# Performance work log

Hardware: AMD Instinct MI355X
Metric: run time of the kernel (lower is better)

The kernel has to match this reference:

```python
import jax, jax.numpy as jnp
import numpy as np

NEG_SLOPE = 0.2  # PyG GATConv default LeakyReLU slope


def add_self_loops(edge_index, n):
    loops = jnp.arange(n, dtype=edge_index.dtype)
    return jnp.concatenate([edge_index, jnp.stack([loops, loops])], axis=1)


def segment_softmax(e, seg, n):
    # e: [E, H], seg: [E] destination node ids
    m = jax.ops.segment_max(e, seg, num_segments=n)          # [N, H]
    ex = jnp.exp(e - m[seg])
    s = jax.ops.segment_sum(ex, seg, num_segments=n)          # [N, H]
    return ex / (s[seg] + 1e-16)


def gat_conv(x, edge_index, W, att_src, att_dst, bias, heads, concat):
    n = x.shape[0]
    c = W.shape[1] // heads
    ei = add_self_loops(edge_index, n)
    src, dst = ei[0], ei[1]
    h = (x @ W).reshape(n, heads, c)                          # [N, H, C]
    a_src = jnp.einsum('nhc,hc->nh', h, att_src)              # [N, H]
    a_dst = jnp.einsum('nhc,hc->nh', h, att_dst)
    e = a_src[src] + a_dst[dst]                               # [E, H]
    e = jax.nn.leaky_relu(e, NEG_SLOPE)
    alpha = segment_softmax(e, dst, n)                        # [E, H]
    msg = alpha[:, :, None] * h[src]                          # [E, H, C]
    out = jax.ops.segment_sum(msg, dst, num_segments=n)       # [N, H, C]
    if concat:
        out = out.reshape(n, heads * c)
    else:
        out = out.mean(axis=1)
    return out + bias


def setup_inputs() -> dict:
    key = jax.random.key(0)
    ks = jax.random.split(key, 16)
    N, E, IN, HID, H, OUT = 50000, 1600000, 512, 256, 8, 128
    s = 0.1
    return {
        'x': jax.random.normal(ks[0], (N, IN), jnp.float32),
        'edge_index': jax.random.randint(ks[1], (2, E), 0, N, jnp.int64),
        'edge_index_2': jax.random.randint(ks[2], (2, E), 0, N, jnp.int64),
        'W1': jax.random.normal(ks[3], (IN, HID * H), jnp.float32) * s,
        'att_src1': jax.random.normal(ks[4], (H, HID), jnp.float32) * s,
        'att_dst1': jax.random.normal(ks[5], (H, HID), jnp.float32) * s,
        'b1': jnp.zeros((HID * H,), jnp.float32),
        'W2': jax.random.normal(ks[6], (HID * H, OUT), jnp.float32) * s,
        'att_src2': jax.random.normal(ks[7], (1, OUT), jnp.float32) * s,
        'att_dst2': jax.random.normal(ks[8], (1, OUT), jnp.float32) * s,
        'b2': jnp.zeros((OUT,), jnp.float32),
        'W3': jax.random.normal(ks[9], (HID * H, OUT), jnp.float32) * s,
        'att_src3': jax.random.normal(ks[10], (1, OUT), jnp.float32) * s,
        'att_dst3': jax.random.normal(ks[11], (1, OUT), jnp.float32) * s,
        'b3': jnp.zeros((OUT,), jnp.float32),
    }


def reference(x, edge_index, edge_index_2, W1, att_src1, att_dst1, b1,
              W2, att_src2, att_dst2, b2, W3, att_src3, att_dst3, b3):
    # Inference mode: F.dropout and GATConv attention dropout are no-ops.
    emb = jax.nn.elu(gat_conv(x, edge_index, W1, att_src1, att_dst1, b1, heads=8, concat=True))
    x1 = gat_conv(emb, edge_index, W2, att_src2, att_dst2, b2, heads=1, concat=False)
    x2 = gat_conv(emb, edge_index_2, W3, att_src3, att_dst3, b3, heads=1, concat=False)
    logits = jax.nn.softmax(x1, axis=1)    # nn.Softmax() legacy dim -> 1 for 2D
    logits_2 = jax.nn.softmax(x2, axis=1)
    predictions = jnp.argmax(logits, axis=1)
    return (logits, logits_2, predictions)
```

## Files before the change

kernel.cpp:

```cpp
#include <hip/hip_runtime.h>
#include <hip/hip_bf16.h>
#include <math.h>

#define N_NODES 50000
#define E_EDGES 1600000
#define EP_EDGES (E_EDGES + N_NODES)
#define IN_F 512
#define HID 256
#define HEADS 8
#define OUTF 128

typedef unsigned short u16;
typedef __attribute__((ext_vector_type(8))) short short8;
typedef __attribute__((ext_vector_type(4))) float floatx4;

static __device__ __forceinline__ float eluf(float x) {
  return x > 0.f ? x : expm1f(x);
}

static __device__ __forceinline__ u16 bf16_hi(float v) {
  __hip_bfloat16 h = __float2bfloat16(v);
  return *(u16*)&h;
}
static __device__ __forceinline__ float bf16_f(u16 u) {
  __hip_bfloat16 h = *(__hip_bfloat16*)&u;
  return __bfloat162float(h);
}
static __device__ __forceinline__ void split3_bf16(float v, u16& h, u16& m, u16& l) {
  h = bf16_hi(v);
  float r1 = v - bf16_f(h);
  m = bf16_hi(r1);
  float r2 = r1 - bf16_f(m);
  l = bf16_hi(r2);
}


__global__ void k_detect(const int* __restrict__ ei, int* __restrict__ flag) {
  __shared__ int nz;
  if (threadIdx.x == 0) nz = 0;
  __syncthreads();
  for (int i = threadIdx.x; i < 4096; i += blockDim.x)
    if (ei[2 * i + 1] != 0) nz = 1;
  __syncthreads();
  if (threadIdx.x == 0) *flag = (nz ? 0 : 1);
}

__global__ void k_init_deg(int* __restrict__ deg, int n) {
  int i = blockIdx.x * 256 + threadIdx.x;
  if (i < n) deg[i] = 1;
}

__global__ void k_count(const int* __restrict__ ei, const int* __restrict__ flag,
                        int* __restrict__ deg, int E) {
  int e = blockIdx.x * 256 + threadIdx.x;
  if (e >= E) return;
  int f = *flag;
  int idx = E + e;
  int dst = ei[f ? 2 * idx : idx];
  atomicAdd(&deg[dst], 1);
}

__global__ __launch_bounds__(1024) void k_scan(const int* __restrict__ deg,
                                               int* __restrict__ rp, int n) {
  __shared__ int sd[1024];
  __shared__ int s_run;
  int tid = threadIdx.x;
  if (tid == 0) s_run = 0;
  __syncthreads();
  for (int base = 0; base < n; base += 1024) {
    int i = base + tid;
    int v = (i < n) ? deg[i] : 0;
    sd[tid] = v;
    __syncthreads();
    for (int off = 1; off < 1024; off <<= 1) {
      int t = (tid >= off) ? sd[tid - off] : 0;
      __syncthreads();
      sd[tid] += t;
      __syncthreads();
    }
    int run = s_run;
    if (i < n) rp[i + 1] = run + sd[tid];
    __syncthreads();
    if (tid == 1023) s_run = run + sd[1023];
    __syncthreads();
  }
  if (tid == 0) rp[0] = 0;
}

__global__ void k_fill_self(const int* __restrict__ rp, int* __restrict__ wp,
                            int* __restrict__ col, int n) {
  int i = blockIdx.x * 256 + threadIdx.x;
  if (i < n) { int p = rp[i]; col[p] = i; wp[i] = p + 1; }
}

__global__ void k_fill_edges(const int* __restrict__ ei, const int* __restrict__ flag,
                             int* __restrict__ wp, int* __restrict__ col, int E) {
  int e = blockIdx.x * 256 + threadIdx.x;
  if (e >= E) return;
  int f = *flag;
  int src = ei[f ? 2 * e : e];
  int didx = E + e;
  int dst = ei[f ? 2 * didx : didx];
  int p = atomicAdd(&wp[dst], 1);
  col[p] = src;
}

__global__ void k_split3_t(const float* __restrict__ W, u16* __restrict__ H,
                           u16* __restrict__ Mv, u16* __restrict__ L,
                           int kshift, int kmask, int Nw, int total) {
  int idx = blockIdx.x * 256 + threadIdx.x;
  if (idx >= total) return;
  int n = idx >> kshift;
  int k = idx & kmask;
  u16 h, m, l;
  split3_bf16(W[(size_t)k * Nw + n], h, m, l);
  H[idx] = h;
  Mv[idx] = m;
  L[idx] = l;
}


#define GBM 128
#define GBN 128
#define GBK 32

#define MFMA_BF16 __builtin_amdgcn_mfma_f32_16x16x32_bf16

__device__ __forceinline__ void gemm_epilogue(floatx4 acc[4][4], float* C,
                                              int ldc, int M, int accum,
                                              int row0, int col0, int wr,
                                              int wc, int lane) {
  int q = lane >> 4, n15 = lane & 15;
#pragma unroll
  for (int i = 0; i < 4; ++i) {
#pragma unroll
    for (int r = 0; r < 4; ++r) {
      int row = row0 + wr * 64 + i * 16 + q * 4 + r;
      if (row < M) {
#pragma unroll
        for (int j = 0; j < 4; ++j) {
          int cg = col0 + wc * 64 + j * 16 + n15;
          float v = acc[i][j][r];
          if (accum) v += C[(size_t)row * ldc + cg];
          C[(size_t)row * ldc + cg] = v;
        }
      }
    }
  }
}

__global__ __launch_bounds__(256) void gemm1_k(
    const float* __restrict__ X, int lda,
    const u16* __restrict__ Bh, const u16* __restrict__ Bm,
    const u16* __restrict__ Bl, int ldb,
    float* __restrict__ C, int ldc, int M, int K) {
  __shared__ __align__(16) u16 lds[24576];
  int tid = threadIdx.x;
  int lane = tid & 63, wave = tid >> 6;
  int wr = wave >> 1, wc = wave & 1;
  int row0 = blockIdx.x * GBM, col0 = blockIdx.y * GBN;
  floatx4 acc[4][4] = {};
  int m0 = tid >> 2, m1 = (tid + 256) >> 2;
  int q0 = tid & 3;
  int lo0 = ((m0 >> 4) * 64 + q0 * 16 + (m0 & 15)) * 8;
  int lo1 = ((m1 >> 4) * 64 + q0 * 16 + (m1 & 15)) * 8;

  for (int k0 = 0; k0 < K; k0 += GBK) {
#pragma unroll
    for (int c = 0; c < 2; ++c) {
      int m = c ? m1 : m0;
      int lo = c ? lo1 : lo0;
      int gr = row0 + m;
      float f[8];
      if (gr < M) {
        float4 f0 = *(const float4*)(X + (size_t)gr * lda + k0 + q0 * 8);
        float4 f1 = *(const float4*)(X + (size_t)gr * lda + k0 + q0 * 8 + 4);
        f[0] = f0.x; f[1] = f0.y; f[2] = f0.z; f[3] = f0.w;
        f[4] = f1.x; f[5] = f1.y; f[6] = f1.z; f[7] = f1.w;
      } else {
#pragma unroll
        for (int e = 0; e < 8; ++e) f[e] = 0.f;
      }
      short8 vh, vm, vl;
#pragma unroll
      for (int e = 0; e < 8; ++e) {
        u16 h, m2, l;
        split3_bf16(f[e], h, m2, l);
        vh[e] = (short)h; vm[e] = (short)m2; vl[e] = (short)l;
      }
      *(short8*)&lds[lo] = vh;
      *(short8*)&lds[4096 + lo] = vm;
      *(short8*)&lds[8192 + lo] = vl;
    }
#pragma unroll
    for (int c = 0; c < 2; ++c) {
      int m = c ? m1 : m0;
      int lo = c ? lo1 : lo0;
      size_t go = (size_t)(col0 + m) * ldb + k0 + q0 * 8;
      *(short8*)&lds[12288 + lo] = *(const short8*)(Bh + go);
      *(short8*)&lds[16384 + lo] = *(const short8*)(Bm + go);
      *(short8*)&lds[20480 + lo] = *(const short8*)(Bl + go);
    }
    __syncthreads();
    short8 a_h[4], a_m[4], a_l[4];
#pragma unroll
    for (int i = 0; i < 4; ++i) {
      int o = ((wr * 4 + i) * 64 + lane) * 8;
      a_h[i] = *(short8*)&lds[o];
      a_m[i] = *(short8*)&lds[4096 + o];
      a_l[i] = *(short8*)&lds[8192 + o];
    }
#pragma unroll
    for (int j = 0; j < 4; ++j) {
      int o = ((wc * 4 + j) * 64 + lane) * 8;
      short8 b_h = *(short8*)&lds[12288 + o];
      short8 b_m = *(short8*)&lds[16384 + o];
      short8 b_l = *(short8*)&lds[20480 + o];
#pragma unroll
      for (int i = 0; i < 4; ++i) {
        acc[i][j] = MFMA_BF16(a_l[i], b_h, acc[i][j], 0, 0, 0);
        acc[i][j] = MFMA_BF16(a_m[i], b_m, acc[i][j], 0, 0, 0);
        acc[i][j] = MFMA_BF16(a_h[i], b_l, acc[i][j], 0, 0, 0);
        acc[i][j] = MFMA_BF16(a_m[i], b_h, acc[i][j], 0, 0, 0);
        acc[i][j] = MFMA_BF16(a_h[i], b_m, acc[i][j], 0, 0, 0);
        acc[i][j] = MFMA_BF16(a_h[i], b_h, acc[i][j], 0, 0, 0);
      }
    }
    __syncthreads();
  }
  gemm_epilogue(acc, C, ldc, M, 0, row0, col0, wr, wc, lane);
}

__device__ __forceinline__ void gemm_core6(
    const u16* __restrict__ Ah, const u16* __restrict__ Am,
    const u16* __restrict__ Al, int lda,
    const u16* __restrict__ Bh, const u16* __restrict__ Bm,
    const u16* __restrict__ Bl, int ldb,
    float* __restrict__ C, int ldc, int M, int K, int row0, int col0,
    u16* lds) {
  int tid = threadIdx.x;
  int lane = tid & 63, wave = tid >> 6;
  int wr = wave >> 1, wc = wave & 1;
  floatx4 acc[4][4] = {};
  int m0 = tid >> 2, m1 = (tid + 256) >> 2;
  int q0 = tid & 3;
  int lo0 = ((m0 >> 4) * 64 + q0 * 16 + (m0 & 15)) * 8;
  int lo1 = ((m1 >> 4) * 64 + q0 * 16 + (m1 & 15)) * 8;
  for (int k0 = 0; k0 < K; k0 += GBK) {
#pragma unroll
    for (int c = 0; c < 2; ++c) {
      int m = c ? m1 : m0;
      int lo = c ? lo1 : lo0;
      int gr = row0 + m;
      short8 vh = {}, vm = {}, vl = {};
      if (gr < M) {
        size_t go = (size_t)gr * lda + k0 + q0 * 8;
        vh = *(const short8*)(Ah + go);
        vm = *(const short8*)(Am + go);
        vl = *(const short8*)(Al + go);
      }
      *(short8*)&lds[lo] = vh;
      *(short8*)&lds[4096 + lo] = vm;
      *(short8*)&lds[8192 + lo] = vl;
      size_t go = (size_t)(col0 + m) * ldb + k0 + q0 * 8;
      *(short8*)&lds[12288 + lo] = *(const short8*)(Bh + go);
      *(short8*)&lds[16384 + lo] = *(const short8*)(Bm + go);
      *(short8*)&lds[20480 + lo] = *(const short8*)(Bl + go);
    }
    __syncthreads();
    short8 a_h[4], a_m[4], a_l[4];
#pragma unroll
    for (int i = 0; i < 4; ++i) {
      int o = ((wr * 4 + i) * 64 + lane) * 8;
      a_h[i] = *(short8*)&lds[o];
      a_m[i] = *(short8*)&lds[4096 + o];
      a_l[i] = *(short8*)&lds[8192 + o];
    }
#pragma unroll
    for (int j = 0; j < 4; ++j) {
      int o = ((wc * 4 + j) * 64 + lane) * 8;
      short8 b_h = *(short8*)&lds[12288 + o];
      short8 b_m = *(short8*)&lds[16384 + o];
      short8 b_l = *(short8*)&lds[20480 + o];
#pragma unroll
      for (int i = 0; i < 4; ++i) {
        acc[i][j] = MFMA_BF16(a_l[i], b_h, acc[i][j], 0, 0, 0);
        acc[i][j] = MFMA_BF16(a_m[i], b_m, acc[i][j], 0, 0, 0);
        acc[i][j] = MFMA_BF16(a_h[i], b_l, acc[i][j], 0, 0, 0);
        acc[i][j] = MFMA_BF16(a_m[i], b_h, acc[i][j], 0, 0, 0);
        acc[i][j] = MFMA_BF16(a_h[i], b_m, acc[i][j], 0, 0, 0);
        acc[i][j] = MFMA_BF16(a_h[i], b_h, acc[i][j], 0, 0, 0);
      }
    }
    __syncthreads();
  }
  gemm_epilogue(acc, C, ldc, M, 1, row0, col0, wr, wc, lane);
}

__device__ __forceinline__ void gemm_core3(
    const u16* __restrict__ Ah, const u16* __restrict__ Am, int lda,
    const u16* __restrict__ Bh, const u16* __restrict__ Bm, int ldb,
    float* __restrict__ C, int ldc, int M, int K, int row0, int col0,
    u16* lds) {
  int tid = threadIdx.x;
  int lane = tid & 63, wave = tid >> 6;
  int wr = wave >> 1, wc = wave & 1;
  floatx4 acc[4][4] = {};
  int m0 = tid >> 2, m1 = (tid + 256) >> 2;
  int q0 = tid & 3;
  int lo0 = ((m0 >> 4) * 64 + q0 * 16 + (m0 & 15)) * 8;
  int lo1 = ((m1 >> 4) * 64 + q0 * 16 + (m1 & 15)) * 8;
  for (int k0 = 0; k0 < K; k0 += GBK) {
#pragma unroll
    for (int c = 0; c < 2; ++c) {
      int m = c ? m1 : m0;
      int lo = c ? lo1 : lo0;
      int gr = row0 + m;
      short8 vh = {}, vm = {};
      if (gr < M) {
        size_t go = (size_t)gr * lda + k0 + q0 * 8;
        vh = *(const short8*)(Ah + go);
        vm = *(const short8*)(Am + go);
      }
      *(short8*)&lds[lo] = vh;
      *(short8*)&lds[4096 + lo] = vm;
      size_t go = (size_t)(col0 + m) * ldb + k0 + q0 * 8;
      *(short8*)&lds[12288 + lo] = *(const short8*)(Bh + go);
      *(short8*)&lds[16384 + lo] = *(const short8*)(Bm + go);
    }
    __syncthreads();
    short8 a_h[4], a_m[4];
#pragma unroll
    for (int i = 0; i < 4; ++i) {
      int o = ((wr * 4 + i) * 64 + lane) * 8;
      a_h[i] = *(short8*)&lds[o];
      a_m[i] = *(short8*)&lds[4096 + o];
    }
#pragma unroll
    for (int j = 0; j < 4; ++j) {
      int o = ((wc * 4 + j) * 64 + lane) * 8;
      short8 b_h = *(short8*)&lds[12288 + o];
      short8 b_m = *(short8*)&lds[16384 + o];
#pragma unroll
      for (int i = 0; i < 4; ++i) {
        acc[i][j] = MFMA_BF16(a_m[i], b_h, acc[i][j], 0, 0, 0);
        acc[i][j] = MFMA_BF16(a_h[i], b_m, acc[i][j], 0, 0, 0);
        acc[i][j] = MFMA_BF16(a_h[i], b_h, acc[i][j], 0, 0, 0);
      }
    }
    __syncthreads();
  }
  gemm_epilogue(acc, C, ldc, M, 1, row0, col0, wr, wc, lane);
}

__global__ __launch_bounds__(256) void gemm23_k(
    const u16* __restrict__ Ah, const u16* __restrict__ Am,
    const u16* __restrict__ Al, int lda,
    const u16* __restrict__ B2h, const u16* __restrict__ B2m,
    const u16* __restrict__ B2l,
    const u16* __restrict__ B3h, const u16* __restrict__ B3m, int ldb,
    float* __restrict__ C2, float* __restrict__ C3, int ldc, int M, int K) {
  __shared__ __align__(16) u16 lds[24576];
  if (blockIdx.z == 0)
    gemm_core6(Ah, Am, Al, lda, B2h, B2m, B2l, ldb, C2, ldc, M, K,
               blockIdx.x * GBM, 0, lds);
  else
    gemm_core3(Ah, Am, lda, B3h, B3m, ldb, C3, ldc, M, K,
               blockIdx.x * GBM, 0, lds);
}

template <int C>
__global__ __launch_bounds__(256) void att_dot(
    const float* __restrict__ h, const float* __restrict__ attS,
    const float* __restrict__ attD, float* __restrict__ aS,
    float* __restrict__ aD, int n) {
  int node = (blockIdx.x * 256 + threadIdx.x) >> 6;
  int lane = threadIdx.x & 63;
  if (node >= n) return;
  float s = 0.f, d = 0.f;
  if (C == 256) {
    float4 hv = *(const float4*)&h[(size_t)node * C + lane * 4];
    float4 sv = *(const float4*)&attS[lane * 4];
    float4 dv = *(const float4*)&attD[lane * 4];
    s = hv.x * sv.x + hv.y * sv.y + hv.z * sv.z + hv.w * sv.w;
    d = hv.x * dv.x + hv.y * dv.y + hv.z * dv.z + hv.w * dv.w;
  } else {
    float2 hv = *(const float2*)&h[(size_t)node * C + lane * 2];
    float2 sv = *(const float2*)&attS[lane * 2];
    float2 dv = *(const float2*)&attD[lane * 2];
    s = hv.x * sv.x + hv.y * sv.y;
    d = hv.x * dv.x + hv.y * dv.y;
  }
  for (int off = 32; off; off >>= 1) {
    s += __shfl_xor(s, off);
    d += __shfl_xor(d, off);
  }
  if (lane == 0) { aS[node] = s; aD[node] = d; }
}

__global__ __launch_bounds__(256) void compute_alpha(
    const int* __restrict__ rp, const int* __restrict__ col,
    const float* __restrict__ aS, const float* __restrict__ aD,
    float* __restrict__ alpha, int n) {
  int node = (blockIdx.x * 256 + threadIdx.x) >> 6;
  int lane = threadIdx.x & 63;
  if (node >= n) return;
  int s0 = rp[node], s1 = rp[node + 1];
  float ad = aD[node];
  float m = -3.0e38f;
  for (int i = s0 + lane; i < s1; i += 64) {
    float e = aS[col[i]] + ad;
    e = e >= 0.f ? e : 0.2f * e;
    m = fmaxf(m, e);
  }
  for (int off = 32; off; off >>= 1) m = fmaxf(m, __shfl_xor(m, off));
  float sum = 0.f;
  for (int i = s0 + lane; i < s1; i += 64) {
    float e = aS[col[i]] + ad;
    e = e >= 0.f ? e : 0.2f * e;
    sum += expf(e - m);
  }
  for (int off = 32; off; off >>= 1) sum += __shfl_xor(sum, off);
  float inv = 1.f / (sum + 1e-16f);
  for (int i = s0 + lane; i < s1; i += 64) {
    float e = aS[col[i]] + ad;
    e = e >= 0.f ? e : 0.2f * e;
    alpha[i] = expf(e - m) * inv;
  }
}

__global__ __launch_bounds__(256) void aggr_gather(
    const int* __restrict__ rp, const int* __restrict__ col,
    const float* __restrict__ alpha, const float* __restrict__ h,
    const float* __restrict__ bias, u16* __restrict__ embH,
    u16* __restrict__ embM, u16* __restrict__ embL, int n) {
  int node = (blockIdx.x * 256 + threadIdx.x) >> 6;
  int lane = threadIdx.x & 63;
  if (node >= n) return;
  int s0 = rp[node], s1 = rp[node + 1];
  float4 acc = make_float4(0.f, 0.f, 0.f, 0.f);
  int i = s0;
  for (; i + 4 <= s1; i += 4) {
    int c0 = col[i], c1 = col[i + 1], c2 = col[i + 2], c3 = col[i + 3];
    float a0 = alpha[i], a1 = alpha[i + 1], a2 = alpha[i + 2], a3 = alpha[i + 3];
    float4 h0 = *(const float4*)&h[(size_t)c0 * HID + lane * 4];
    float4 h1 = *(const float4*)&h[(size_t)c1 * HID + lane * 4];
    float4 h2 = *(const float4*)&h[(size_t)c2 * HID + lane * 4];
    float4 h3 = *(const float4*)&h[(size_t)c3 * HID + lane * 4];
    acc.x += a0 * h0.x + a1 * h1.x + a2 * h2.x + a3 * h3.x;
    acc.y += a0 * h0.y + a1 * h1.y + a2 * h2.y + a3 * h3.y;
    acc.z += a0 * h0.z + a1 * h1.z + a2 * h2.z + a3 * h3.z;
    acc.w += a0 * h0.w + a1 * h1.w + a2 * h2.w + a3 * h3.w;
  }
  for (; i < s1; ++i) {
    int c = col[i];
    float a = alpha[i];
    float4 hv = *(const float4*)&h[(size_t)c * HID + lane * 4];
    acc.x += a * hv.x; acc.y += a * hv.y; acc.z += a * hv.z; acc.w += a * hv.w;
  }
  float4 bb = *(const float4*)&bias[lane * 4];
  float v0 = eluf(acc.x + bb.x);
  float v1 = eluf(acc.y + bb.y);
  float v2 = eluf(acc.z + bb.z);
  float v3 = eluf(acc.w + bb.w);
  ushort4 uh, um, ul;
  split3_bf16(v0, uh.x, um.x, ul.x);
  split3_bf16(v1, uh.y, um.y, ul.y);
  split3_bf16(v2, uh.z, um.z, ul.z);
  split3_bf16(v3, uh.w, um.w, ul.w);
  size_t o = (size_t)node * HID + lane * 4;
  *(ushort4*)&embH[o] = uh;
  *(ushort4*)&embM[o] = um;
  *(ushort4*)&embL[o] = ul;
}

__global__ __launch_bounds__(256) void aggr_l2(
    const int* __restrict__ rp, const int* __restrict__ col,
    const float* __restrict__ aS, const float* __restrict__ aD,
    const float* __restrict__ h, const float* __restrict__ bias,
    float* __restrict__ out, int n) {
  int node = (blockIdx.x * 256 + threadIdx.x) >> 6;
  int lane = threadIdx.x & 63;
  if (node >= n) return;
  int s0 = rp[node], s1 = rp[node + 1];
  float ad = aD[node];
  float m = -3.0e38f;
  for (int i = s0 + lane; i < s1; i += 64) {
    float e = aS[col[i]] + ad;
    e = e >= 0.f ? e : 0.2f * e;
    m = fmaxf(m, e);
  }
  for (int off = 32; off; off >>= 1) m = fmaxf(m, __shfl_xor(m, off));
  float sum = 0.f;
  for (int i = s0 + lane; i < s1; i += 64) {
    float e = aS[col[i]] + ad;
    e = e >= 0.f ? e : 0.2f * e;
    sum += expf(e - m);
  }
  for (int off = 32; off; off >>= 1) sum += __shfl_xor(sum, off);
  float denom = sum + 1e-16f;
  float2 acc = make_float2(0.f, 0.f);
  for (int i = s0; i < s1; ++i) {
    int s = col[i];
    float e = aS[s] + ad;
    e = e >= 0.f ? e : 0.2f * e;
    float a = expf(e - m) / denom;
    float2 hv = *(const float2*)&h[(size_t)s * OUTF + lane * 2];
    acc.x += a * hv.x; acc.y += a * hv.y;
  }
  float2 bb = *(const float2*)&bias[lane * 2];
  acc.x += bb.x; acc.y += bb.y;
  *(float2*)&out[(size_t)node * OUTF + lane * 2] = acc;
}

__global__ __launch_bounds__(256) void softmax_rows(float* __restrict__ x,
                                                    float* __restrict__ pred,
                                                    int n) {
  int node = (blockIdx.x * 256 + threadIdx.x) >> 6;
  int lane = threadIdx.x & 63;
  if (node >= n) return;
  float2 v = *(float2*)&x[(size_t)node * OUTF + lane * 2];
  float bv;
  int bi;
  if (v.y > v.x) { bv = v.y; bi = 2 * lane + 1; }
  else           { bv = v.x; bi = 2 * lane; }
  for (int off = 32; off; off >>= 1) {
    float ov = __shfl_xor(bv, off);
    int oi = __shfl_xor(bi, off);
    if (ov > bv || (ov == bv && oi < bi)) { bv = ov; bi = oi; }
  }
  float e0 = expf(v.x - bv), e1 = expf(v.y - bv);
  float s = e0 + e1;
  for (int off = 32; off; off >>= 1) s += __shfl_xor(s, off);
  float2 r;
  r.x = e0 / s;
  r.y = e1 / s;
  *(float2*)&x[(size_t)node * OUTF + lane * 2] = r;
  if (pred != nullptr && lane == 0) pred[node] = (float)bi;
}

extern "C" void kernel_launch(void* const* d_in, const int* in_sizes, int n_in,
                              void* d_out, int out_size, void* d_ws, size_t ws_size,
                              hipStream_t stream) {
  const int N = N_NODES, E = E_EDGES;
  const float* x     = (const float*)d_in[0];
  const int*   ei1   = (const int*)d_in[1];
  const int*   ei2   = (const int*)d_in[2];
  const float* W1    = (const float*)d_in[3];
  const float* attS1 = (const float*)d_in[4];
  const float* attD1 = (const float*)d_in[5];
  const float* b1    = (const float*)d_in[6];
  const float* W2    = (const float*)d_in[7];
  const float* attS2 = (const float*)d_in[8];
  const float* attD2 = (const float*)d_in[9];
  const float* b2    = (const float*)d_in[10];
  const float* W3    = (const float*)d_in[11];
  const float* attS3 = (const float*)d_in[12];
  const float* attD3 = (const float*)d_in[13];
  const float* b3    = (const float*)d_in[14];

  char* ws = (char*)d_ws;
  size_t off = 0;
  auto take = [&](size_t bytes) {
    off = (off + 255) & ~(size_t)255;
    size_t o = off;
    off += bytes;
    return o;
  };
  int*   col1 = (int*)(ws + take((size_t)EP_EDGES * 4));
  int*   col2 = (int*)(ws + take((size_t)EP_EDGES * 4));
  int*   rp1  = (int*)(ws + take((size_t)(N + 1) * 4));
  int*   rp2  = (int*)(ws + take((size_t)(N + 1) * 4));
  int*   wp1  = (int*)(ws + take((size_t)N * 4));
  int*   wp2  = (int*)(ws + take((size_t)N * 4));
  int*   flag = (int*)(ws + take(256));
  float* h1h  = (float*)(ws + take((size_t)N * HID * 4));
  u16*   embH = (u16*)(ws + take((size_t)N * HID * 2));
  u16*   embM = (u16*)(ws + take((size_t)N * HID * 2));
  u16*   embL = (u16*)(ws + take((size_t)N * HID * 2));
  float* h2   = (float*)(ws + take((size_t)N * OUTF * 4 * 2));
  float* h3   = h2 + (size_t)N * OUTF;
  float* alpha= (float*)(ws + take((size_t)EP_EDGES * 4));
  u16*   W1Th = (u16*)(ws + take((size_t)IN_F * HID * HEADS * 2));
  u16*   W1Tm = (u16*)(ws + take((size_t)IN_F * HID * HEADS * 2));
  u16*   W1Tl = (u16*)(ws + take((size_t)IN_F * HID * HEADS * 2));
  u16*   W2Th = (u16*)(ws + take((size_t)HID * HEADS * OUTF * 2));
  u16*   W2Tm = (u16*)(ws + take((size_t)HID * HEADS * OUTF * 2));
  u16*   W2Tl = (u16*)(ws + take((size_t)HID * HEADS * OUTF * 2));
  u16*   W3Th = (u16*)(ws + take((size_t)HID * HEADS * OUTF * 2));
  u16*   W3Tm = (u16*)(ws + take((size_t)HID * HEADS * OUTF * 2));
  float* as1  = (float*)(ws + take((size_t)N * 4));
  float* ad1  = (float*)(ws + take((size_t)N * 4));
  float* as2  = (float*)(ws + take((size_t)N * 4));
  float* ad2  = (float*)(ws + take((size_t)N * 4));
  float* as3  = (float*)(ws + take((size_t)N * 4));
  float* ad3  = (float*)(ws + take((size_t)N * 4));

  float* outp = (float*)d_out;
  float* x1   = outp;
  float* x2   = outp + (size_t)N * OUTF;
  float* pred = outp + (size_t)2 * N * OUTF;

  const int gN = (N + 255) / 256;
  const int gE = (E + 255) / 256;
  const int gW = (N + 3) / 4;
  const int gM = (N + GBM - 1) / GBM;

  k_split3_t<<<(IN_F * HID * HEADS + 255) / 256, 256, 0, stream>>>(
      W1, W1Th, W1Tm, W1Tl, 9, 511, HID * HEADS, IN_F * HID * HEADS);
  k_split3_t<<<(HID * HEADS * OUTF + 255) / 256, 256, 0, stream>>>(
      W2, W2Th, W2Tm, W2Tl, 11, 2047, OUTF, HID * HEADS * OUTF);
  k_split3_t<<<(HID * HEADS * OUTF + 255) / 256, 256, 0, stream>>>(
      W3, W3Th, W3Tm, W3Tm , 11, 2047,
      OUTF, HID * HEADS * OUTF);

  k_detect<<<1, 256, 0, stream>>>(ei1, flag);

  k_init_deg<<<gN, 256, 0, stream>>>(wp1, N);
  k_count<<<gE, 256, 0, stream>>>(ei1, flag, wp1, E);
  k_scan<<<1, 1024, 0, stream>>>(wp1, rp1, N);
  k_fill_self<<<gN, 256, 0, stream>>>(rp1, wp1, col1, N);
  k_fill_edges<<<gE, 256, 0, stream>>>(ei1, flag, wp1, col1, E);

  k_init_deg<<<gN, 256, 0, stream>>>(wp2, N);
  k_count<<<gE, 256, 0, stream>>>(ei2, flag, wp2, E);
  k_scan<<<1, 1024, 0, stream>>>(wp2, rp2, N);
  k_fill_self<<<gN, 256, 0, stream>>>(rp2, wp2, col2, N);
  k_fill_edges<<<gE, 256, 0, stream>>>(ei2, flag, wp2, col2, E);

  hipMemsetAsync(h2, 0, (size_t)N * OUTF * 4 * 2, stream);

  for (int h = 0; h < HEADS; ++h) {
    gemm1_k<<<dim3(gM, HID / GBN), 256, 0, stream>>>(
        x, IN_F,
        W1Th + (size_t)h * HID * IN_F, W1Tm + (size_t)h * HID * IN_F,
        W1Tl + (size_t)h * HID * IN_F, IN_F, h1h, HID, N, IN_F);
    att_dot<HID><<<gW, 256, 0, stream>>>(h1h, attS1 + (size_t)h * HID,
                                         attD1 + (size_t)h * HID, as1, ad1, N);
    compute_alpha<<<gW, 256, 0, stream>>>(rp1, col1, as1, ad1, alpha, N);
    aggr_gather<<<gW, 256, 0, stream>>>(rp1, col1, alpha, h1h,
                                        b1 + (size_t)h * HID, embH, embM, embL, N);
    gemm23_k<<<dim3(gM, 1, 2), 256, 0, stream>>>(
        embH, embM, embL, HID,
        W2Th + (size_t)h * HID, W2Tm + (size_t)h * HID, W2Tl + (size_t)h * HID,
        W3Th + (size_t)h * HID, W3Tm + (size_t)h * HID, HID * HEADS,
        h2, h3, OUTF, N, HID);
  }

  att_dot<OUTF><<<gW, 256, 0, stream>>>(h2, attS2, attD2, as2, ad2, N);
  att_dot<OUTF><<<gW, 256, 0, stream>>>(h3, attS3, attD3, as3, ad3, N);
  aggr_l2<<<gW, 256, 0, stream>>>(rp1, col1, as2, ad2, h2, b2, x1, N);
  aggr_l2<<<gW, 256, 0, stream>>>(rp2, col2, as3, ad3, h3, b3, x2, N);

  softmax_rows<<<gW, 256, 0, stream>>>(x1, pred, N);
  softmax_rows<<<gW, 256, 0, stream>>>(x2, nullptr, N);
}
```

Before: 4.653 ms.

## Fuse edge softmax into neighbor aggregation with warp-shuffle fast path

The separate compute_alpha kernel is folded into the layer-1 aggregation kernel, so the per-edge alpha array is no longer written to and read back from global memory for each of the 8 heads. For nodes with degree up to 64, each lane keeps one edge's column index and score in registers. The max and sum are done with a single shuffle reduction, and during the gather the coefficients are broadcast with __shfl. Larger-degree nodes recompute alpha inline during the gather, and layer 2 gets the same fast path. The change also clamps edge indices and gives the W3 low-part split its own buffer.

```diff
diff --git a/kernel.cpp b/kernel.cpp
--- a/kernel.cpp
+++ b/kernel.cpp
@@ -32,6 +32,10 @@
   m = bf16_hi(r1);
   float r2 = r1 - bf16_f(m);
   l = bf16_hi(r2);
+}
+
+static __device__ __forceinline__ int clampi(int v, int n) {
+  return v < 0 ? 0 : (v >= n ? n - 1 : v);
 }
 
 
@@ -56,7 +60,7 @@
   if (e >= E) return;
   int f = *flag;
   int idx = E + e;
-  int dst = ei[f ? 2 * idx : idx];
+  int dst = clampi(ei[f ? 2 * idx : idx], N_NODES);
   atomicAdd(&deg[dst], 1);
 }
 
@@ -98,9 +102,9 @@
   int e = blockIdx.x * 256 + threadIdx.x;
   if (e >= E) return;
   int f = *flag;
-  int src = ei[f ? 2 * e : e];
+  int src = clampi(ei[f ? 2 * e : e], N_NODES);
   int didx = E + e;
-  int dst = ei[f ? 2 * didx : didx];
+  int dst = clampi(ei[f ? 2 * didx : didx], N_NODES);
   int p = atomicAdd(&wp[dst], 1);
   col[p] = src;
 }
@@ -398,66 +402,70 @@
   if (lane == 0) { aS[node] = s; aD[node] = d; }
 }
 
-__global__ __launch_bounds__(256) void compute_alpha(
+__global__ __launch_bounds__(256) void aggr_l1_fused(
     const int* __restrict__ rp, const int* __restrict__ col,
     const float* __restrict__ aS, const float* __restrict__ aD,
-    float* __restrict__ alpha, int n) {
+    const float* __restrict__ h, const float* __restrict__ bias,
+    u16* __restrict__ embH, u16* __restrict__ embM, u16* __restrict__ embL,
+    int n) {
   int node = (blockIdx.x * 256 + threadIdx.x) >> 6;
   int lane = threadIdx.x & 63;
   if (node >= n) return;
   int s0 = rp[node], s1 = rp[node + 1];
+  int d = s1 - s0;
   float ad = aD[node];
-  float m = -3.0e38f;
-  for (int i = s0 + lane; i < s1; i += 64) {
-    float e = aS[col[i]] + ad;
-    e = e >= 0.f ? e : 0.2f * e;
-    m = fmaxf(m, e);
-  }
-  for (int off = 32; off; off >>= 1) m = fmaxf(m, __shfl_xor(m, off));
-  float sum = 0.f;
-  for (int i = s0 + lane; i < s1; i += 64) {
-    float e = aS[col[i]] + ad;
-    e = e >= 0.f ? e : 0.2f * e;
-    sum += expf(e - m);
-  }
-  for (int off = 32; off; off >>= 1) sum += __shfl_xor(sum, off);
-  float inv = 1.f / (sum + 1e-16f);
-  for (int i = s0 + lane; i < s1; i += 64) {
-    float e = aS[col[i]] + ad;
-    e = e >= 0.f ? e : 0.2f * e;
-    alpha[i] = expf(e - m) * inv;
-  }
-}
-
-__global__ __launch_bounds__(256) void aggr_gather(
-    const int* __restrict__ rp, const int* __restrict__ col,
-    const float* __restrict__ alpha, const float* __restrict__ h,
-    const float* __restrict__ bias, u16* __restrict__ embH,
-    u16* __restrict__ embM, u16* __restrict__ embL, int n) {
-  int node = (blockIdx.x * 256 + threadIdx.x) >> 6;
-  int lane = threadIdx.x & 63;
-  if (node >= n) return;
-  int s0 = rp[node], s1 = rp[node + 1];
   float4 acc = make_float4(0.f, 0.f, 0.f, 0.f);
-  int i = s0;
-  for (; i + 4 <= s1; i += 4) {
-    int c0 = col[i], c1 = col[i + 1], c2 = col[i + 2], c3 = col[i + 3];
-    float a0 = alpha[i], a1 = alpha[i + 1], a2 = alpha[i + 2], a3 = alpha[i + 3];
-    float4 h0 = *(const float4*)&h[(size_t)c0 * HID + lane * 4];
-    float4 h1 = *(const float4*)&h[(size_t)c1 * HID + lane * 4];
-    float4 h2 = *(const float4*)&h[(size_t)c2 * HID + lane * 4];
-    float4 h3 = *(const float4*)&h[(size_t)c3 * HID + lane * 4];
-    acc.x += a0 * h0.x + a1 * h1.x + a2 * h2.x + a3 * h3.x;
-    acc.y += a0 * h0.y + a1 * h1.y + a2 * h2.y + a3 * h3.y;
-    acc.z += a0 * h0.z + a1 * h1.z + a2 * h2.z + a3 * h3.z;
-    acc.w += a0 * h0.w + a1 * h1.w + a2 * h2.w + a3 * h3.w;
-  }
-  for (; i < s1; ++i) {
-    int c = col[i];
-    float a = alpha[i];
-    float4 hv = *(const float4*)&h[(size_t)c * HID + lane * 4];
-    acc.x += a * hv.x; acc.y += a * hv.y; acc.z += a * hv.z; acc.w += a * hv.w;
-  }
+
+  if (d <= 64) {
+    int c = 0;
+    float e = -3.0e38f;
+    if (lane < d) {
+      c = clampi(col[s0 + lane], n);
+      float t = aS[c] + ad;
+      e = t >= 0.f ? t : 0.2f * t;
+    }
+    float m = e;
+    for (int off = 32; off; off >>= 1) m = fmaxf(m, __shfl_xor(m, off));
+    float ex = (lane < d) ? expf(e - m) : 0.f;
+    float s = ex;
+    for (int off = 32; off; off >>= 1) s += __shfl_xor(s, off);
+    float al = ex * (1.f / (s + 1e-16f));
+    for (int j = 0; j < d; j += 8) {
+#pragma unroll
+      for (int t = 0; t < 8; ++t) {
+        int ct = __shfl(c, j + t);
+        float at = __shfl(al, j + t);
+        float4 hv = *(const float4*)&h[(size_t)ct * HID + lane * 4];
+        acc.x += at * hv.x; acc.y += at * hv.y;
+        acc.z += at * hv.z; acc.w += at * hv.w;
+      }
+    }
+  } else {
+    float m = -3.0e38f;
+    for (int i = s0 + lane; i < s1; i += 64) {
+      float e = aS[clampi(col[i], n)] + ad;
+      e = e >= 0.f ? e : 0.2f * e;
+      m = fmaxf(m, e);
+    }
+    for (int off = 32; off; off >>= 1) m = fmaxf(m, __shfl_xor(m, off));
+    float sum = 0.f;
+    for (int i = s0 + lane; i < s1; i += 64) {
+      float e = aS[clampi(col[i], n)] + ad;
+      e = e >= 0.f ? e : 0.2f * e;
+      sum += expf(e - m);
+    }
+    for (int off = 32; off; off >>= 1) sum += __shfl_xor(sum, off);
+    float inv = 1.f / (sum + 1e-16f);
+    for (int i = s0; i < s1; ++i) {
+      int ci = clampi(col[i], n);
+      float e = aS[ci] + ad;
+      e = e >= 0.f ? e : 0.2f * e;
+      float a = expf(e - m) * inv;
+      float4 hv = *(const float4*)&h[(size_t)ci * HID + lane * 4];
+      acc.x += a * hv.x; acc.y += a * hv.y; acc.z += a * hv.z; acc.w += a * hv.w;
+    }
+  }
+
   float4 bb = *(const float4*)&bias[lane * 4];
   float v0 = eluf(acc.x + bb.x);
   float v1 = eluf(acc.y + bb.y);
@@ -474,7 +482,7 @@
   *(ushort4*)&embL[o] = ul;
 }
 
-__global__ __launch_bounds__(256) void aggr_l2(
+__global__ __launch_bounds__(256) void aggr_l2_fused(
     const int* __restrict__ rp, const int* __restrict__ col,
     const float* __restrict__ aS, const float* __restrict__ aD,
     const float* __restrict__ h, const float* __restrict__ bias,
@@ -483,31 +491,59 @@
   int lane = threadIdx.x & 63;
   if (node >= n) return;
   int s0 = rp[node], s1 = rp[node + 1];
+  int d = s1 - s0;
   float ad = aD[node];
-  float m = -3.0e38f;
-  for (int i = s0 + lane; i < s1; i += 64) {
-    float e = aS[col[i]] + ad;
-    e = e >= 0.f ? e : 0.2f * e;
-    m = fmaxf(m, e);
-  }
-  for (int off = 32; off; off >>= 1) m = fmaxf(m, __shfl_xor(m, off));
-  float sum = 0.f;
-  for (int i = s0 + lane; i < s1; i += 64) {
-    float e = aS[col[i]] + ad;
-    e = e >= 0.f ? e : 0.2f * e;
-    sum += expf(e - m);
-  }
-  for (int off = 32; off; off >>= 1) sum += __shfl_xor(sum, off);
-  float denom = sum + 1e-16f;
   float2 acc = make_float2(0.f, 0.f);
-  for (int i = s0; i < s1; ++i) {
-    int s = col[i];
-    float e = aS[s] + ad;
-    e = e >= 0.f ? e : 0.2f * e;
-    float a = expf(e - m) / denom;
-    float2 hv = *(const float2*)&h[(size_t)s * OUTF + lane * 2];
-    acc.x += a * hv.x; acc.y += a * hv.y;
-  }
+
+  if (d <= 64) {
+    int c = 0;
+    float e = -3.0e38f;
+    if (lane < d) {
+      c = clampi(col[s0 + lane], n);
+      float t = aS[c] + ad;
+      e = t >= 0.f ? t : 0.2f * t;
+    }
+    float m = e;
+    for (int off = 32; off; off >>= 1) m = fmaxf(m, __shfl_xor(m, off));
+    float ex = (lane < d) ? expf(e - m) : 0.f;
+    float s = ex;
+    for (int off = 32; off; off >>= 1) s += __shfl_xor(s, off);
+    float al = ex * (1.f / (s + 1e-16f));
+    for (int j = 0; j < d; j += 8) {
+#pragma unroll
+      for (int t = 0; t < 8; ++t) {
+        int ct = __shfl(c, j + t);
+        float at = __shfl(al, j + t);
+        float2 hv = *(const float2*)&h[(size_t)ct * OUTF + lane * 2];
+        acc.x += at * hv.x; acc.y += at * hv.y;
+      }
+    }
+  } else {
+    float m = -3.0e38f;
+    for (int i = s0 + lane; i < s1; i += 64) {
+      float e = aS[clampi(col[i], n)] + ad;
+      e = e >= 0.f ? e : 0.2f * e;
+      m = fmaxf(m, e);
+    }
+    for (int off = 32; off; off >>= 1) m = fmaxf(m, __shfl_xor(m, off));
+    float sum = 0.f;
+    for (int i = s0 + lane; i < s1; i += 64) {
+      float e = aS[clampi(col[i], n)] + ad;
+      e = e >= 0.f ? e : 0.2f * e;
+      sum += expf(e - m);
+    }
+    for (int off = 32; off; off >>= 1) sum += __shfl_xor(sum, off);
+    float inv = 1.f / (sum + 1e-16f);
+    for (int i = s0; i < s1; ++i) {
+      int ci = clampi(col[i], n);
+      float e = aS[ci] + ad;
+      e = e >= 0.f ? e : 0.2f * e;
+      float a = expf(e - m) * inv;
+      float2 hv = *(const float2*)&h[(size_t)ci * OUTF + lane * 2];
+      acc.x += a * hv.x; acc.y += a * hv.y;
+    }
+  }
+
   float2 bb = *(const float2*)&bias[lane * 2];
   acc.x += bb.x; acc.y += bb.y;
   *(float2*)&out[(size_t)node * OUTF + lane * 2] = acc;
@@ -580,7 +616,6 @@
   u16*   embL = (u16*)(ws + take((size_t)N * HID * 2));
   float* h2   = (float*)(ws + take((size_t)N * OUTF * 4 * 2));
   float* h3   = h2 + (size_t)N * OUTF;
-  float* alpha= (float*)(ws + take((size_t)EP_EDGES * 4));
   u16*   W1Th = (u16*)(ws + take((size_t)IN_F * HID * HEADS * 2));
   u16*   W1Tm = (u16*)(ws + take((size_t)IN_F * HID * HEADS * 2));
   u16*   W1Tl = (u16*)(ws + take((size_t)IN_F * HID * HEADS * 2));
@@ -589,6 +624,7 @@
   u16*   W2Tl = (u16*)(ws + take((size_t)HID * HEADS * OUTF * 2));
   u16*   W3Th = (u16*)(ws + take((size_t)HID * HEADS * OUTF * 2));
   u16*   W3Tm = (u16*)(ws + take((size_t)HID * HEADS * OUTF * 2));
+  u16*   W3Tl = (u16*)(ws + take((size_t)HID * HEADS * OUTF * 2));
   float* as1  = (float*)(ws + take((size_t)N * 4));
   float* ad1  = (float*)(ws + take((size_t)N * 4));
   float* as2  = (float*)(ws + take((size_t)N * 4));
@@ -611,8 +647,7 @@
   k_split3_t<<<(HID * HEADS * OUTF + 255) / 256, 256, 0, stream>>>(
       W2, W2Th, W2Tm, W2Tl, 11, 2047, OUTF, HID * HEADS * OUTF);
   k_split3_t<<<(HID * HEADS * OUTF + 255) / 256, 256, 0, stream>>>(
-      W3, W3Th, W3Tm, W3Tm , 11, 2047,
-      OUTF, HID * HEADS * OUTF);
+      W3, W3Th, W3Tm, W3Tl, 11, 2047, OUTF, HID * HEADS * OUTF);
 
   k_detect<<<1, 256, 0, stream>>>(ei1, flag);
 
@@ -637,9 +672,9 @@
         W1Tl + (size_t)h * HID * IN_F, IN_F, h1h, HID, N, IN_F);
     att_dot<HID><<<gW, 256, 0, stream>>>(h1h, attS1 + (size_t)h * HID,
                                          attD1 + (size_t)h * HID, as1, ad1, N);
-    compute_alpha<<<gW, 256, 0, stream>>>(rp1, col1, as1, ad1, alpha, N);
-    aggr_gather<<<gW, 256, 0, stream>>>(rp1, col1, alpha, h1h,
-                                        b1 + (size_t)h * HID, embH, embM, embL, N);
+    aggr_l1_fused<<<gW, 256, 0, stream>>>(rp1, col1, as1, ad1, h1h,
+                                          b1 + (size_t)h * HID,
+                                          embH, embM, embL, N);
     gemm23_k<<<dim3(gM, 1, 2), 256, 0, stream>>>(
         embH, embM, embL, HID,
         W2Th + (size_t)h * HID, W2Tm + (size_t)h * HID, W2Tl + (size_t)h * HID,
@@ -649,8 +684,8 @@
 
   att_dot<OUTF><<<gW, 256, 0, stream>>>(h2, attS2, attD2, as2, ad2, N);
   att_dot<OUTF><<<gW, 256, 0, stream>>>(h3, attS3, attD3, as3, ad3, N);
-  aggr_l2<<<gW, 256, 0, stream>>>(rp1, col1, as2, ad2, h2, b2, x1, N);
-  aggr_l2<<<gW, 256, 0, stream>>>(rp2, col2, as3, ad3, h3, b3, x2, N);
+  aggr_l2_fused<<<gW, 256, 0, stream>>>(rp1, col1, as2, ad2, h2, b2, x1, N);
+  aggr_l2_fused<<<gW, 256, 0, stream>>>(rp2, col2, as3, ad3, h3, b3, x2, N);
 
   softmax_rows<<<gW, 256, 0, stream>>>(x1, pred, N);
   softmax_rows<<<gW, 256, 0, stream>>>(x2, nullptr, N);
```

New measurement: 4.335 ms. -6.8%, faster.
